# Performance work log

Hardware: AMD Instinct MI355X
Metric: run time of the kernel (lower is better)

Reference implementation:

```python
import jax, jax.numpy as jnp
import numpy as np

TEMP = 0.05
EPS = 1e-8  # torch CosineSimilarity eps


def setup_inputs() -> dict:
    key = jax.random.key(0)
    k1, k2 = jax.random.split(key)
    feature1 = jax.random.normal(k1, (4096, 768), dtype=jnp.float32)
    feature2 = jax.random.normal(k2, (4096, 768), dtype=jnp.float32)
    return {"feature1": feature1, "feature2": feature2}


def reference(feature1, feature2):
    # cosine similarity via L2-normalize + GEMM (same math as broadcast cos_sim)
    n1 = feature1 / jnp.maximum(jnp.linalg.norm(feature1, axis=-1, keepdims=True), EPS)
    n2 = feature2 / jnp.maximum(jnp.linalg.norm(feature2, axis=-1, keepdims=True), EPS)
    logits = jnp.einsum("id,jd->ij", n1, n2) / TEMP  # [N, N]
    # cross-entropy with labels = arange(N) -> mean of -log_softmax diagonal
    logp = jax.nn.log_softmax(logits, axis=-1)
    loss = -jnp.mean(jnp.diagonal(logp))
    return loss
```

## Files before the change

### kernel.cpp

```cpp
#include <hip/hip_runtime.h>
#include <hip/hip_bf16.h>

#define NROWS 4096
#define DIM   768
#define NKT   12

typedef __attribute__((ext_vector_type(8))) short short8;
typedef __attribute__((ext_vector_type(4))) float f32x4;

#define GAS(p) ((const __attribute__((address_space(1))) void*)(p))
#define SAS(p) ((__attribute__((address_space(3))) void*)(p))

__device__ __forceinline__ unsigned short f2bf(float x) {
    unsigned int u = __builtin_bit_cast(unsigned int, x);
    u += 0x7fffu + ((u >> 16) & 1u);
    return (unsigned short)(u >> 16);
}

__global__ __launch_bounds__(256) void k_norm(const float* __restrict__ f1,
                                              const float* __restrict__ f2,
                                              unsigned short* __restrict__ n1,
                                              unsigned short* __restrict__ n2,
                                              float* __restrict__ rowsum) {
    int b = blockIdx.x;
    int wid = threadIdx.x >> 6, lane = threadIdx.x & 63;
    int rowidx = b * 4 + wid;
    const float* src = (rowidx < NROWS) ? f1 : f2;
    unsigned short* dst = (rowidx < NROWS) ? n1 : n2;
    int row = rowidx & (NROWS - 1);
    const float4* srow = (const float4*)(src + (size_t)row * DIM);
    float4 v[3];
    float ss = 0.f;
#pragma unroll
    for (int r = 0; r < 3; ++r) {
        v[r] = srow[lane + 64 * r];
        ss += v[r].x * v[r].x + v[r].y * v[r].y + v[r].z * v[r].z + v[r].w * v[r].w;
    }
#pragma unroll
    for (int off = 32; off; off >>= 1) ss += __shfl_xor(ss, off);
    float inv = 1.0f / fmaxf(sqrtf(ss), 1e-8f);
    ushort4* drow = (ushort4*)(dst + (size_t)row * DIM);
#pragma unroll
    for (int r = 0; r < 3; ++r) {
        ushort4 o;
        o.x = f2bf(v[r].x * inv);
        o.y = f2bf(v[r].y * inv);
        o.z = f2bf(v[r].z * inv);
        o.w = f2bf(v[r].w * inv);
        drow[lane + 64 * r] = o;
    }
    if (b == 0) {
        float4 z = {0.f, 0.f, 0.f, 0.f};
#pragma unroll
        for (int i = 0; i < 4; ++i) ((float4*)rowsum)[threadIdx.x + 256 * i] = z;
    }
}


#define BARRIER __builtin_amdgcn_s_barrier()
#define WAIT_LGKM0 do { asm volatile("s_waitcnt lgkmcnt(0)" ::: "memory"); \
                        __builtin_amdgcn_sched_barrier(0); } while (0)
#define WAIT_VM8   do { asm volatile("s_waitcnt vmcnt(8)" ::: "memory"); \
                        __builtin_amdgcn_sched_barrier(0); } while (0)
#define PRIO1 __builtin_amdgcn_s_setprio(1)
#define PRIO0 __builtin_amdgcn_s_setprio(0)

__global__ __launch_bounds__(256, 2) void k_gemm_lse(const unsigned short* __restrict__ n1,
                                                     const unsigned short* __restrict__ n2,
                                                     float* __restrict__ rowsum,
                                                     float* __restrict__ diag) {
    __shared__ alignas(16) char ldsbuf[65536];
    char* ldsc = (char*)ldsbuf;

    int wg = blockIdx.x;
    int swz = (wg & 7) * 128 + (wg >> 3);
    int bi = swz >> 5;
    int bj = swz & 31;

    int tid = threadIdx.x;
    int wid = tid >> 6;
    int lane = tid & 63;
    int l15 = lane & 15, lk = lane >> 4;
    int wr = wid >> 1, wc = wid & 1;

    const unsigned short* abase = n1 + (size_t)bi * 128 * DIM;
    const unsigned short* bbase = n2 + (size_t)bj * 128 * DIM;

    const int stoff = (tid >> 3) * DIM + (((tid & 7) ^ ((tid >> 3) & 7)) * 8);

    const int swzl = (lane & 7) << 4;
    const int lko0 = l15 * 128 + ((lk * 16) ^ swzl);
    const int lko1 = l15 * 128 + (((64 + lk * 16)) ^ swzl);

    char* LAp[2] = { ldsc + wr * 8192,          ldsc + 32768 + wr * 8192 };
    char* LBp[2] = { ldsc + 16384 + wc * 8192,  ldsc + 32768 + 16384 + wc * 8192 };

#define STG1(b, isB, base, chunk, kt) do { \
    const unsigned short* _s = (base) + ((chunk) * 32) * DIM + (kt) * 64 + stoff; \
    char* _d = ldsc + (b) * 32768 + (isB) * 16384 + (chunk) * 4096 + tid * 16; \
    __builtin_amdgcn_global_load_lds(GAS(_s), SAS(_d), 16, 0, 0); \
} while (0)

#define STG8(b, kt) do { \
    STG1(b, 0, abase, 0, kt); STG1(b, 0, abase, 1, kt); \
    STG1(b, 0, abase, 2, kt); STG1(b, 0, abase, 3, kt); \
    STG1(b, 1, bbase, 0, kt); STG1(b, 1, bbase, 1, kt); \
    STG1(b, 1, bbase, 2, kt); STG1(b, 1, bbase, 3, kt); \
} while (0)

#define LDA2(b, q, areg) do { _Pragma("unroll") for (int m = 0; m < 2; ++m) { \
    const char* _p = LAp[b] + ((q) * 32 + m * 16) * 128; \
    areg[m][0] = *(const short8*)(_p + lko0); \
    areg[m][1] = *(const short8*)(_p + lko1); } } while (0)

#define LDB4(b, breg) do { _Pragma("unroll") for (int n = 0; n < 4; ++n) { \
    const char* _p = LBp[b] + n * 16 * 128; \
    breg[n][0] = *(const short8*)(_p + lko0); \
    breg[n][1] = *(const short8*)(_p + lko1); } } while (0)

#define MMH(qm, areg, breg) do { _Pragma("unroll") for (int m = 0; m < 2; ++m) \
    _Pragma("unroll") for (int n = 0; n < 4; ++n) { \
    f32x4* _c = &acc[(qm) * 2 + m][n]; \
    *_c = __builtin_amdgcn_mfma_f32_16x16x32_bf16(areg[m][0], breg[n][0], *_c, 0, 0, 0); \
    *_c = __builtin_amdgcn_mfma_f32_16x16x32_bf16(areg[m][1], breg[n][1], *_c, 0, 0, 0); } } while (0)

    short8 a0A[2][2], a1A[2][2], aB[2][2], b0[4][2], b1[4][2];
    f32x4 acc[4][4] = {};

    STG8(0, 0);
    STG8(1, 1);
    WAIT_VM8;
    BARRIER;
    LDA2(0, 0, a0A); LDB4(0, b0);

    for (int t = 0; t < NKT; t += 2) {
        int t2 = (t + 2 < NKT) ? t + 2 : t + 2 - NKT;
        int t3 = (t + 3 < NKT) ? t + 3 : t + 3 - NKT;
        WAIT_LGKM0;
        LDA2(0, 1, aB);
        PRIO1; MMH(0, a0A, b0); PRIO0;
        WAIT_LGKM0;
        BARRIER;
        STG8(0, t2);
        PRIO1; MMH(1, aB, b0); PRIO0;
        WAIT_VM8;
        LDA2(1, 0, a1A); LDB4(1, b1);
        BARRIER;
        WAIT_LGKM0;
        LDA2(1, 1, aB);
        PRIO1; MMH(0, a1A, b1); PRIO0;
        WAIT_LGKM0;
        BARRIER;
        STG8(1, t3);
        PRIO1; MMH(1, aB, b1); PRIO0;
        WAIT_VM8;
        LDA2(0, 0, a0A); LDB4(0, b0);
        BARRIER;
    }

    __syncthreads();

    const bool dblk = (bi == bj);
    const int rowb = bi * 128 + wr * 64;
    const int colb = bj * 128 + wc * 64;
#pragma unroll
    for (int mi = 0; mi < 4; ++mi) {
#pragma unroll
        for (int r = 0; r < 4; ++r) {
            float s = 0.f;
            int gi = rowb + mi * 16 + lk * 4 + r;
#pragma unroll
            for (int ni = 0; ni < 4; ++ni) {
                float v = acc[mi][ni][r] * 20.0f;
                s += __expf(v);
                if (dblk) {
                    int gj = colb + ni * 16 + l15;
                    if (gi == gj) diag[gi] = v;
                }
            }
#pragma unroll
            for (int off = 1; off < 16; off <<= 1) s += __shfl_xor(s, off);
            if (l15 == 0) atomicAdd(rowsum + gi, s);
        }
    }
}

__global__ __launch_bounds__(1024) void k_final(const float* __restrict__ rowsum,
                                                const float* __restrict__ diag,
                                                float* __restrict__ out) {
    int tid = threadIdx.x;
    float s = 0.f;
#pragma unroll
    for (int i = 0; i < 4; ++i) {
        int idx = tid + 1024 * i;
        s += logf(rowsum[idx]) - diag[idx];
    }
#pragma unroll
    for (int off = 32; off; off >>= 1) s += __shfl_xor(s, off);
    __shared__ float red[16];
    if ((tid & 63) == 0) red[tid >> 6] = s;
    __syncthreads();
    if (tid == 0) {
        float tot = 0.f;
#pragma unroll
        for (int i = 0; i < 16; ++i) tot += red[i];
        out[0] = tot * (1.0f / NROWS);
    }
}

extern "C" void kernel_launch(void* const* d_in, const int* in_sizes, int n_in,
                              void* d_out, int out_size, void* d_ws, size_t ws_size,
                              hipStream_t stream) {
    const float* f1 = (const float*)d_in[0];
    const float* f2 = (const float*)d_in[1];
    float* out = (float*)d_out;

    char* ws = (char*)d_ws;
    unsigned short* n1 = (unsigned short*)ws;
    unsigned short* n2 = n1 + (size_t)NROWS * DIM;
    float* rowsum = (float*)(ws + 2 * (size_t)NROWS * DIM * sizeof(unsigned short));
    float* diag = rowsum + NROWS;

    k_norm<<<2048, 256, 0, stream>>>(f1, f2, n1, n2, rowsum);
    k_gemm_lse<<<1024, 256, 0, stream>>>(n1, n2, rowsum, diag);
    k_final<<<1, 1024, 0, stream>>>(rowsum, diag, out);
}
```

Baseline: 113.0 us.

## Quantize normalized features to FP8 and use fp8 MFMA for the similarity GEMM

The normalization kernel now writes rows scaled by 8 as packed FP8 (e4m3) bytes instead of bf16. The GEMM loads 128-wide K tiles of bytes, which halves the K iterations, and issues fp8 16x16x32 MFMAs, undoing the scale with 1/64 in the epilogue. The aim is to halve global and LDS traffic and double matrix throughput. In exchange the logits lose precision, which after the x20 temperature scaling may push the loss past the tolerance.

```diff
diff --git a/kernel.cpp b/kernel.cpp
--- a/kernel.cpp
+++ b/kernel.cpp
@@ -3,30 +3,23 @@
 
 #define NROWS 4096
 #define DIM   768
-#define NKT   12
-
-typedef __attribute__((ext_vector_type(8))) short short8;
+#define NKT   6
+
 typedef __attribute__((ext_vector_type(4))) float f32x4;
 
 #define GAS(p) ((const __attribute__((address_space(1))) void*)(p))
 #define SAS(p) ((__attribute__((address_space(3))) void*)(p))
 
-__device__ __forceinline__ unsigned short f2bf(float x) {
-    unsigned int u = __builtin_bit_cast(unsigned int, x);
-    u += 0x7fffu + ((u >> 16) & 1u);
-    return (unsigned short)(u >> 16);
-}
-
 __global__ __launch_bounds__(256) void k_norm(const float* __restrict__ f1,
                                               const float* __restrict__ f2,
-                                              unsigned short* __restrict__ n1,
-                                              unsigned short* __restrict__ n2,
+                                              unsigned char* __restrict__ n1,
+                                              unsigned char* __restrict__ n2,
                                               float* __restrict__ rowsum) {
     int b = blockIdx.x;
     int wid = threadIdx.x >> 6, lane = threadIdx.x & 63;
     int rowidx = b * 4 + wid;
     const float* src = (rowidx < NROWS) ? f1 : f2;
-    unsigned short* dst = (rowidx < NROWS) ? n1 : n2;
+    unsigned char* dst = (rowidx < NROWS) ? n1 : n2;
     int row = rowidx & (NROWS - 1);
     const float4* srow = (const float4*)(src + (size_t)row * DIM);
     float4 v[3];
@@ -38,16 +31,13 @@
     }
 #pragma unroll
     for (int off = 32; off; off >>= 1) ss += __shfl_xor(ss, off);
-    float inv = 1.0f / fmaxf(sqrtf(ss), 1e-8f);
-    ushort4* drow = (ushort4*)(dst + (size_t)row * DIM);
+    float inv8 = 8.0f / fmaxf(sqrtf(ss), 1e-8f);
+    unsigned int* drow = (unsigned int*)(dst + (size_t)row * DIM);
 #pragma unroll
     for (int r = 0; r < 3; ++r) {
-        ushort4 o;
-        o.x = f2bf(v[r].x * inv);
-        o.y = f2bf(v[r].y * inv);
-        o.z = f2bf(v[r].z * inv);
-        o.w = f2bf(v[r].w * inv);
-        drow[lane + 64 * r] = o;
+        int w = __builtin_amdgcn_cvt_pk_fp8_f32(v[r].x * inv8, v[r].y * inv8, 0, false);
+        w = __builtin_amdgcn_cvt_pk_fp8_f32(v[r].z * inv8, v[r].w * inv8, w, true);
+        drow[lane + 64 * r] = (unsigned int)w;
     }
     if (b == 0) {
         float4 z = {0.f, 0.f, 0.f, 0.f};
@@ -65,8 +55,8 @@
 #define PRIO1 __builtin_amdgcn_s_setprio(1)
 #define PRIO0 __builtin_amdgcn_s_setprio(0)
 
-__global__ __launch_bounds__(256, 2) void k_gemm_lse(const unsigned short* __restrict__ n1,
-                                                     const unsigned short* __restrict__ n2,
+__global__ __launch_bounds__(256, 2) void k_gemm_lse(const unsigned char* __restrict__ n1,
+                                                     const unsigned char* __restrict__ n2,
                                                      float* __restrict__ rowsum,
                                                      float* __restrict__ diag) {
     __shared__ alignas(16) char ldsbuf[65536];
@@ -83,20 +73,22 @@
     int l15 = lane & 15, lk = lane >> 4;
     int wr = wid >> 1, wc = wid & 1;
 
-    const unsigned short* abase = n1 + (size_t)bi * 128 * DIM;
-    const unsigned short* bbase = n2 + (size_t)bj * 128 * DIM;
-
-    const int stoff = (tid >> 3) * DIM + (((tid & 7) ^ ((tid >> 3) & 7)) * 8);
-
-    const int swzl = (lane & 7) << 4;
-    const int lko0 = l15 * 128 + ((lk * 16) ^ swzl);
-    const int lko1 = l15 * 128 + (((64 + lk * 16)) ^ swzl);
+    const unsigned char* abase = n1 + (size_t)bi * 128 * DIM;
+    const unsigned char* bbase = n2 + (size_t)bj * 128 * DIM;
+
+    const int stoff = (tid >> 3) * DIM + (((tid & 7) ^ ((tid >> 3) & 7)) * 16);
+
+    const int h7 = l15 & 7;
+    const int fbase = l15 * 128 + (lk & 1) * 8;
+    int slotx[4];
+#pragma unroll
+    for (int j = 0; j < 4; ++j) slotx[j] = ((2 * j + (lk >> 1)) ^ h7) * 16;
 
     char* LAp[2] = { ldsc + wr * 8192,          ldsc + 32768 + wr * 8192 };
     char* LBp[2] = { ldsc + 16384 + wc * 8192,  ldsc + 32768 + 16384 + wc * 8192 };
 
 #define STG1(b, isB, base, chunk, kt) do { \
-    const unsigned short* _s = (base) + ((chunk) * 32) * DIM + (kt) * 64 + stoff; \
+    const unsigned char* _s = (base) + ((chunk) * 32) * DIM + (kt) * 128 + stoff; \
     char* _d = ldsc + (b) * 32768 + (isB) * 16384 + (chunk) * 4096 + tid * 16; \
     __builtin_amdgcn_global_load_lds(GAS(_s), SAS(_d), 16, 0, 0); \
 } while (0)
@@ -108,53 +100,51 @@
     STG1(b, 1, bbase, 2, kt); STG1(b, 1, bbase, 3, kt); \
 } while (0)
 
-#define LDA2(b, q, areg) do { _Pragma("unroll") for (int m = 0; m < 2; ++m) { \
-    const char* _p = LAp[b] + ((q) * 32 + m * 16) * 128; \
-    areg[m][0] = *(const short8*)(_p + lko0); \
-    areg[m][1] = *(const short8*)(_p + lko1); } } while (0)
-
-#define LDB4(b, breg) do { _Pragma("unroll") for (int n = 0; n < 4; ++n) { \
-    const char* _p = LBp[b] + n * 16 * 128; \
-    breg[n][0] = *(const short8*)(_p + lko0); \
-    breg[n][1] = *(const short8*)(_p + lko1); } } while (0)
-
-#define MMH(qm, areg, breg) do { _Pragma("unroll") for (int m = 0; m < 2; ++m) \
-    _Pragma("unroll") for (int n = 0; n < 4; ++n) { \
-    f32x4* _c = &acc[(qm) * 2 + m][n]; \
-    *_c = __builtin_amdgcn_mfma_f32_16x16x32_bf16(areg[m][0], breg[n][0], *_c, 0, 0, 0); \
-    *_c = __builtin_amdgcn_mfma_f32_16x16x32_bf16(areg[m][1], breg[n][1], *_c, 0, 0, 0); } } while (0)
-
-    short8 a0A[2][2], a1A[2][2], aB[2][2], b0[4][2], b1[4][2];
+#define LDF(b, jp, Areg, Breg) do { \
+    _Pragma("unroll") for (int m = 0; m < 4; ++m) \
+    _Pragma("unroll") for (int jj = 0; jj < 2; ++jj) { \
+        Areg[m][jj] = *(const long*)(LAp[b] + m * 2048 + fbase + slotx[(jp) * 2 + jj]); \
+        Breg[m][jj] = *(const long*)(LBp[b] + m * 2048 + fbase + slotx[(jp) * 2 + jj]); \
+    } } while (0)
+
+#define MM32(Areg, Breg) do { _Pragma("unroll") for (int m = 0; m < 4; ++m) \
+    _Pragma("unroll") for (int n = 0; n < 4; ++n) \
+    _Pragma("unroll") for (int jj = 0; jj < 2; ++jj) { \
+    f32x4* _c = &acc[m][n]; \
+    *_c = __builtin_amdgcn_mfma_f32_16x16x32_fp8_fp8(Areg[m][jj], Breg[n][jj], *_c, 0, 0, 0); \
+    } } while (0)
+
+    long A0[4][2], B0[4][2], A1[4][2], B1[4][2];
     f32x4 acc[4][4] = {};
 
     STG8(0, 0);
     STG8(1, 1);
     WAIT_VM8;
     BARRIER;
-    LDA2(0, 0, a0A); LDB4(0, b0);
+    LDF(0, 0, A0, B0);
 
     for (int t = 0; t < NKT; t += 2) {
         int t2 = (t + 2 < NKT) ? t + 2 : t + 2 - NKT;
         int t3 = (t + 3 < NKT) ? t + 3 : t + 3 - NKT;
         WAIT_LGKM0;
-        LDA2(0, 1, aB);
-        PRIO1; MMH(0, a0A, b0); PRIO0;
+        LDF(0, 1, A1, B1);
+        PRIO1; MM32(A0, B0); PRIO0;
         WAIT_LGKM0;
         BARRIER;
         STG8(0, t2);
-        PRIO1; MMH(1, aB, b0); PRIO0;
+        PRIO1; MM32(A1, B1); PRIO0;
         WAIT_VM8;
-        LDA2(1, 0, a1A); LDB4(1, b1);
-        BARRIER;
-        WAIT_LGKM0;
-        LDA2(1, 1, aB);
-        PRIO1; MMH(0, a1A, b1); PRIO0;
+        LDF(1, 0, A0, B0);
+        BARRIER;
+        WAIT_LGKM0;
+        LDF(1, 1, A1, B1);
+        PRIO1; MM32(A0, B0); PRIO0;
         WAIT_LGKM0;
         BARRIER;
         STG8(1, t3);
-        PRIO1; MMH(1, aB, b1); PRIO0;
+        PRIO1; MM32(A1, B1); PRIO0;
         WAIT_VM8;
-        LDA2(0, 0, a0A); LDB4(0, b0);
+        LDF(0, 0, A0, B0);
         BARRIER;
     }
 
@@ -171,7 +161,7 @@
             int gi = rowb + mi * 16 + lk * 4 + r;
 #pragma unroll
             for (int ni = 0; ni < 4; ++ni) {
-                float v = acc[mi][ni][r] * 20.0f;
+                float v = acc[mi][ni][r] * (20.0f / 64.0f);
                 s += __expf(v);
                 if (dblk) {
                     int gj = colb + ni * 16 + l15;
@@ -216,9 +206,9 @@
     float* out = (float*)d_out;
 
     char* ws = (char*)d_ws;
-    unsigned short* n1 = (unsigned short*)ws;
-    unsigned short* n2 = n1 + (size_t)NROWS * DIM;
-    float* rowsum = (float*)(ws + 2 * (size_t)NROWS * DIM * sizeof(unsigned short));
+    unsigned char* n1 = (unsigned char*)ws;
+    unsigned char* n2 = n1 + (size_t)NROWS * DIM;
+    float* rowsum = (float*)(ws + 2 * (size_t)NROWS * DIM);
     float* diag = rowsum + NROWS;
 
     k_norm<<<2048, 256, 0, stream>>>(f1, f2, n1, n2, rowsum);
```

Measured after the change: 109.7 us. 3.0% less time.
